# Kernel optimization log

Hardware: AMD Instinct MI355X
Metric: run time of the kernel (lower is better)

Reference implementation:

```python
import jax, jax.numpy as jnp
import numpy as np

ALPHA = 0.2  # LeakyReLU negative slope
NEG_INF = -9e15


def setup_inputs() -> dict:
    key = jax.random.key(0)
    k1, k2, k3, k4 = jax.random.split(key, 4)
    B, T, N, F_in, F_out = 8, 8, 1024, 64, 64
    h = jax.random.normal(k1, (B, T, N, F_in), dtype=jnp.float32)
    adj = jax.random.randint(k2, (B, T, N, N), 0, 2, dtype=jnp.int32)
    # xavier_uniform with gain=1.414
    def xavier(k, shape, gain=1.414):
        fan_in, fan_out = shape[0], shape[1]
        bound = gain * np.sqrt(6.0 / (fan_in + fan_out))
        return jax.random.uniform(k, shape, jnp.float32, -bound, bound)
    W = xavier(k3, (F_in, F_out))
    a = xavier(k4, (2 * F_out, 1))
    return {"h": h, "adj": adj, "W": W, "a": a}


def reference(h, adj, W, a):
    # h: [B,T,N,F_in], adj: [B,T,N,N], W: [F_in,F_out], a: [2*F_out,1]
    F_out = W.shape[1]
    Wh = h @ W  # [B,T,N,F_out]
    a1 = a[:F_out, 0]   # source half
    a2 = a[F_out:, 0]   # target half
    s1 = Wh @ a1        # [B,T,N]
    s2 = Wh @ a2        # [B,T,N]
    # e[...,i,j] = LeakyReLU(s1_i + s2_j)  == original concat-linear score
    e = jax.nn.leaky_relu(s1[..., :, None] + s2[..., None, :], negative_slope=ALPHA)
    att = jnp.where(adj > 0, e, NEG_INF)
    att = jax.nn.softmax(att, axis=-1)  # [B,T,N,N]
    # dropout omitted: reference runs in eval mode (p only active in training)
    h_prime = att @ Wh  # [B,T,N,F_out]
    return jax.nn.elu(h_prime)  # concat=True path
```

## Files before the change

kernel.cpp:

```cpp
#include <hip/hip_runtime.h>

#define NN 1024
#define FF 64
#define NBT 64
#define INV_LN2 1.44269504088896f

typedef float f32x4 __attribute__((ext_vector_type(4)));
typedef short s16x8 __attribute__((ext_vector_type(8)));

__device__ __forceinline__ short f2bf(float f) {
    unsigned u = __builtin_bit_cast(unsigned, f);
    u = (u + 0x7FFFu + ((u >> 16) & 1u)) >> 16;
    return (short)u;
}

__global__ __launch_bounds__(256) void k1(const float* __restrict__ h,
                                          const float* __restrict__ W,
                                          const float* __restrict__ a,
                                          short* __restrict__ WhT,
                                          float* __restrict__ s1g,
                                          float* __restrict__ s2g) {
    __shared__ float Wl[64 * 64];
    __shared__ float al[128];
    __shared__ float s1sh[128], s2sh[128];
    const int blk = blockIdx.x;
    const int bt = blk >> 3;
    const int rbase = (blk & 7) * 128;
    const int t = threadIdx.x;

    for (int i = t; i < 1024; i += 256)
        ((f32x4*)Wl)[i] = ((const f32x4*)W)[i];
    if (t < 32) ((f32x4*)al)[t] = ((const f32x4*)a)[t];
    __syncthreads();

    const int row = rbase + (t & 127);
    const int half = t >> 7;
    const float* hrow = h + ((size_t)bt * NN + row) * FF;
    float hv[64];
#pragma unroll
    for (int i = 0; i < 16; i++)
        ((f32x4*)hv)[i] = ((const f32x4*)hrow)[i];

    float s1 = 0.f, s2 = 0.f;
    short* wt = WhT + (size_t)bt * FF * NN + row;
#pragma unroll
    for (int cgi = 0; cgi < 8; cgi++) {
        const int cg = half * 8 + cgi;
        f32x4 acc = {0.f, 0.f, 0.f, 0.f};
#pragma unroll
        for (int k = 0; k < 64; k++) {
            f32x4 w4 = ((const f32x4*)Wl)[k * 16 + cg];
            acc += hv[k] * w4;
        }
        const int c0 = cg * 4;
        s1 += acc.x * al[c0] + acc.y * al[c0 + 1] + acc.z * al[c0 + 2] + acc.w * al[c0 + 3];
        s2 += acc.x * al[64 + c0] + acc.y * al[64 + c0 + 1] + acc.z * al[64 + c0 + 2] + acc.w * al[64 + c0 + 3];
        wt[(size_t)(c0 + 0) * NN] = f2bf(acc.x);
        wt[(size_t)(c0 + 1) * NN] = f2bf(acc.y);
        wt[(size_t)(c0 + 2) * NN] = f2bf(acc.z);
        wt[(size_t)(c0 + 3) * NN] = f2bf(acc.w);
    }
    if (half == 1) { s1sh[t & 127] = s1; s2sh[t & 127] = s2; }
    __syncthreads();
    if (half == 0) {
        s1g[bt * NN + row] = (s1 + s1sh[t]) * INV_LN2;
        s2g[bt * NN + row] = (s2 + s2sh[t]) * INV_LN2;
    }
}

__global__ __launch_bounds__(256) void k2(const int* __restrict__ adj,
                                          const short* __restrict__ WhT,
                                          const float* __restrict__ s1g,
                                          const float* __restrict__ s2g,
                                          float* __restrict__ out) {
    __shared__ __align__(16) short Pa[2][64 * 40];
    __shared__ __align__(16) short Pw[2][64 * 40];
    __shared__ float s2l[NN];

    const int bxl = blockIdx.x;
    const int bx = (bxl & 7) * 128 + (bxl >> 3);
    const int bt = bx >> 4;
    const int ibase = (bx & 15) * 64;
    const int t = threadIdx.x;

    ((f32x4*)s2l)[t] = ((const f32x4*)(s2g + (size_t)bt * NN))[t];

    const int r = t >> 2;
    const int jc = (t & 3) * 8;
    const float s1v = s1g[bt * NN + ibase + r];

    const int* adjp = adj + ((size_t)bt * NN + ibase + r) * NN + jc;
    const short* whp = WhT + (size_t)bt * FF * NN + (size_t)r * NN + jc;

    const int wv = t >> 6;
    const int l = t & 63;
    const int m = l & 15;
    const int q = l >> 4;
    const int foff = (wv * 16 + m) * 40 + q * 8;
    const int boff0 = (0 * 16 + m) * 40 + q * 8;
    const int boff1 = (1 * 16 + m) * 40 + q * 8;
    const int boff2 = (2 * 16 + m) * 40 + q * 8;
    const int boff3 = (3 * 16 + m) * 40 + q * 8;

    f32x4 acc0 = {0.f, 0.f, 0.f, 0.f};
    f32x4 acc1 = {0.f, 0.f, 0.f, 0.f};
    f32x4 acc2 = {0.f, 0.f, 0.f, 0.f};
    f32x4 acc3 = {0.f, 0.f, 0.f, 0.f};
    f32x4 accR = {0.f, 0.f, 0.f, 0.f};
    const s16x8 ones = {0x3F80, 0x3F80, 0x3F80, 0x3F80, 0x3F80, 0x3F80, 0x3F80, 0x3F80};

    int4 ca0 = *(const int4*)(adjp);
    int4 ca1 = *(const int4*)(adjp + 4);
    int4 cw  = *(const int4*)(whp);

    __syncthreads();

    for (int jt = 0; jt < 32; jt++) {
        const int b = jt & 1;

        int aj[8] = {ca0.x, ca0.y, ca0.z, ca0.w, ca1.x, ca1.y, ca1.z, ca1.w};
        f32x4 s2a = *(const f32x4*)&s2l[jt * 32 + jc];
        f32x4 s2b = *(const f32x4*)&s2l[jt * 32 + jc + 4];
        float sv[8] = {s2a.x, s2a.y, s2a.z, s2a.w, s2b.x, s2b.y, s2b.z, s2b.w};
        s16x8 pbv;
#pragma unroll
        for (int u = 0; u < 8; u++) {
            float e = s1v + sv[u];
            e = fmaxf(e, 0.2f * e);
            e = fminf(e, 86.f);
            float p = (aj[u] > 0) ? exp2f(e) : 0.f;
            pbv[u] = f2bf(p);
        }
        *(s16x8*)&Pa[b][r * 40 + jc] = pbv;
        *(int4*)&Pw[b][r * 40 + jc] = cw;
        __syncthreads();

        const int jn = (jt < 31 ? jt + 1 : 31) * 32;
        int4 na0 = *(const int4*)(adjp + jn);
        int4 na1 = *(const int4*)(adjp + jn + 4);
        int4 nw  = *(const int4*)(whp + jn);

        s16x8 af = *(const s16x8*)&Pa[b][foff];
        acc0 = __builtin_amdgcn_mfma_f32_16x16x32_bf16(af, *(const s16x8*)&Pw[b][boff0], acc0, 0, 0, 0);
        acc1 = __builtin_amdgcn_mfma_f32_16x16x32_bf16(af, *(const s16x8*)&Pw[b][boff1], acc1, 0, 0, 0);
        acc2 = __builtin_amdgcn_mfma_f32_16x16x32_bf16(af, *(const s16x8*)&Pw[b][boff2], acc2, 0, 0, 0);
        acc3 = __builtin_amdgcn_mfma_f32_16x16x32_bf16(af, *(const s16x8*)&Pw[b][boff3], acc3, 0, 0, 0);
        accR = __builtin_amdgcn_mfma_f32_16x16x32_bf16(af, ones, accR, 0, 0, 0);

        ca0 = na0; ca1 = na1; cw = nw;
    }

    float rinv[4];
#pragma unroll
    for (int e = 0; e < 4; e++)
        rinv[e] = accR[e] > 0.f ? 1.f / accR[e] : 0.f;

    float* outp = out + ((size_t)bt * NN + ibase + wv * 16 + q * 4) * FF + m;
#pragma unroll
    for (int e = 0; e < 4; e++) {
        float v0 = acc0[e] * rinv[e];
        float v1 = acc1[e] * rinv[e];
        float v2 = acc2[e] * rinv[e];
        float v3 = acc3[e] * rinv[e];
        v0 = v0 > 0.f ? v0 : expm1f(v0);
        v1 = v1 > 0.f ? v1 : expm1f(v1);
        v2 = v2 > 0.f ? v2 : expm1f(v2);
        v3 = v3 > 0.f ? v3 : expm1f(v3);
        float* o = outp + (size_t)e * FF;
        o[0]  = v0;
        o[16] = v1;
        o[32] = v2;
        o[48] = v3;
    }
}

extern "C" void kernel_launch(void* const* d_in, const int* in_sizes, int n_in,
                              void* d_out, int out_size, void* d_ws, size_t ws_size,
                              hipStream_t stream) {
    const float* h  = (const float*)d_in[0];
    const int*  adj = (const int*)d_in[1];
    const float* W  = (const float*)d_in[2];
    const float* a  = (const float*)d_in[3];
    float* out = (float*)d_out;

    short* WhT = (short*)d_ws;
    float* s1  = (float*)((char*)d_ws + (size_t)NBT * FF * NN * 2);
    float* s2  = s1 + NBT * NN;

    k1<<<512, 256, 0, stream>>>(h, W, a, WhT, s1, s2);
    k2<<<1024, 256, 0, stream>>>(adj, WhT, s1, s2, out);
}
```

Before: 415.5 us.

## Pack adjacency into bitmasks in a pre-pass kernel before attention

Adds a new kernel k0 that reads the int32 adjacency matrix once and uses wave ballots to pack it into 64-bit bitmasks in workspace. The attention kernel k2 then loads each block's 64x1024 mask slice into LDS up front and tests bits instead of streaming eight int32 adjacency values per thread per tile. This takes the large adjacency stream and its registers out of k2's main loop. The cost is an extra kernel launch and a pass over the full adjacency tensor that no longer overlaps with k2's MFMA work. The mask now tests adj != 0 rather than adj > 0, which gives the same result for 0/1 inputs.

```diff
diff --git a/kernel.cpp b/kernel.cpp
--- a/kernel.cpp
+++ b/kernel.cpp
@@ -12,6 +12,26 @@
     unsigned u = __builtin_bit_cast(unsigned, f);
     u = (u + 0x7FFFu + ((u >> 16) & 1u)) >> 16;
     return (short)u;
+}
+
+__global__ __launch_bounds__(256) void k0(const int* __restrict__ adj,
+                                          unsigned long long* __restrict__ adjb) {
+    const int wid = (blockIdx.x << 2) | (threadIdx.x >> 6);
+    const int l = threadIdx.x & 63;
+    const int row0 = wid * 16;
+    for (int i = 0; i < 16; i++) {
+        const int row = row0 + i;
+        const int* rp = adj + (size_t)row * NN + l;
+        unsigned long long keep = 0;
+#pragma unroll
+        for (int it = 0; it < 16; it++) {
+            int v = rp[it * 64];
+            unsigned long long bal = __ballot(v != 0);
+            if (l == it) keep = bal;
+        }
+        if (l < 16)
+            adjb[(size_t)row * 16 + l] = keep;
+    }
 }
 
 __global__ __launch_bounds__(256) void k1(const float* __restrict__ h,
@@ -68,7 +88,7 @@
     }
 }
 
-__global__ __launch_bounds__(256) void k2(const int* __restrict__ adj,
+__global__ __launch_bounds__(256) void k2(const unsigned* __restrict__ adjb,
                                           const short* __restrict__ WhT,
                                           const float* __restrict__ s1g,
                                           const float* __restrict__ s2g,
@@ -76,6 +96,7 @@
     __shared__ __align__(16) short Pa[2][64 * 40];
     __shared__ __align__(16) short Pw[2][64 * 40];
     __shared__ float s2l[NN];
+    __shared__ unsigned ml[64][36];
 
     const int bxl = blockIdx.x;
     const int bx = (bxl & 7) * 128 + (bxl >> 3);
@@ -89,7 +110,14 @@
     const int jc = (t & 3) * 8;
     const float s1v = s1g[bt * NN + ibase + r];
 
-    const int* adjp = adj + ((size_t)bt * NN + ibase + r) * NN + jc;
+    {
+        const unsigned* gb = adjb + ((size_t)bt * NN + ibase + r) * 32 + (t & 3) * 8;
+        int4 g0 = ((const int4*)gb)[0];
+        int4 g1 = ((const int4*)gb)[1];
+        *(int4*)&ml[r][(t & 3) * 8]     = g0;
+        *(int4*)&ml[r][(t & 3) * 8 + 4] = g1;
+    }
+
     const short* whp = WhT + (size_t)bt * FF * NN + (size_t)r * NN + jc;
 
     const int wv = t >> 6;
@@ -109,16 +137,14 @@
     f32x4 accR = {0.f, 0.f, 0.f, 0.f};
     const s16x8 ones = {0x3F80, 0x3F80, 0x3F80, 0x3F80, 0x3F80, 0x3F80, 0x3F80, 0x3F80};
 
-    int4 ca0 = *(const int4*)(adjp);
-    int4 ca1 = *(const int4*)(adjp + 4);
-    int4 cw  = *(const int4*)(whp);
+    int4 cw = *(const int4*)(whp);
 
     __syncthreads();
 
     for (int jt = 0; jt < 32; jt++) {
         const int b = jt & 1;
 
-        int aj[8] = {ca0.x, ca0.y, ca0.z, ca0.w, ca1.x, ca1.y, ca1.z, ca1.w};
+        const unsigned mb = (ml[r][jt] >> jc) & 255u;
         f32x4 s2a = *(const f32x4*)&s2l[jt * 32 + jc];
         f32x4 s2b = *(const f32x4*)&s2l[jt * 32 + jc + 4];
         float sv[8] = {s2a.x, s2a.y, s2a.z, s2a.w, s2b.x, s2b.y, s2b.z, s2b.w};
@@ -128,7 +154,7 @@
             float e = s1v + sv[u];
             e = fmaxf(e, 0.2f * e);
             e = fminf(e, 86.f);
-            float p = (aj[u] > 0) ? exp2f(e) : 0.f;
+            float p = (mb & (1u << u)) ? exp2f(e) : 0.f;
             pbv[u] = f2bf(p);
         }
         *(s16x8*)&Pa[b][r * 40 + jc] = pbv;
@@ -136,9 +162,7 @@
         __syncthreads();
 
         const int jn = (jt < 31 ? jt + 1 : 31) * 32;
-        int4 na0 = *(const int4*)(adjp + jn);
-        int4 na1 = *(const int4*)(adjp + jn + 4);
-        int4 nw  = *(const int4*)(whp + jn);
+        int4 nw = *(const int4*)(whp + jn);
 
         s16x8 af = *(const s16x8*)&Pa[b][foff];
         acc0 = __builtin_amdgcn_mfma_f32_16x16x32_bf16(af, *(const s16x8*)&Pw[b][boff0], acc0, 0, 0, 0);
@@ -147,7 +171,7 @@
         acc3 = __builtin_amdgcn_mfma_f32_16x16x32_bf16(af, *(const s16x8*)&Pw[b][boff3], acc3, 0, 0, 0);
         accR = __builtin_amdgcn_mfma_f32_16x16x32_bf16(af, ones, accR, 0, 0, 0);
 
-        ca0 = na0; ca1 = na1; cw = nw;
+        cw = nw;
     }
 
     float rinv[4];
@@ -186,7 +210,10 @@
     short* WhT = (short*)d_ws;
     float* s1  = (float*)((char*)d_ws + (size_t)NBT * FF * NN * 2);
     float* s2  = s1 + NBT * NN;
-
+    unsigned long long* adjb =
+        (unsigned long long*)((char*)d_ws + 8 * 1024 * 1024 + 512 * 1024);
+
+    k0<<<1024, 256, 0, stream>>>(adj, adjb);
     k1<<<512, 256, 0, stream>>>(h, W, a, WhT, s1, s2);
-    k2<<<1024, 256, 0, stream>>>(adj, WhT, s1, s2, out);
-}
+    k2<<<1024, 256, 0, stream>>>((const unsigned*)adjb, WhT, s1, s2, out);
+}
```

Result: slower. 436.7 us (+5.1%).
